# Kernel tuning notes

Hardware: AMD Instinct MI355X
Metric: run time of the kernel (lower is better)

Reference implementation:

```python
import jax, jax.numpy as jnp
import numpy as np

DIM = 256
HEAD_DIM = 64
NH = DIM // HEAD_DIM
PS = 2  # fine patch size
EPS = 1e-5


def _conv(x, w, b, stride, pad):
    y = jax.lax.conv_general_dilated(x, w, (stride, stride), ((pad, pad), (pad, pad)),
                                     dimension_numbers=('NCHW', 'OIHW', 'NCHW'))
    return y + b[None, :, None, None]


def _bn(x, g, b, m, v):
    s = g * jax.lax.rsqrt(v + EPS)
    return x * s[None, :, None, None] + (b - m * s)[None, :, None, None]


def setup_inputs() -> dict:
    key = jax.random.key(0)
    ks = jax.random.split(key, 24)
    C = DIM
    d = {}
    d['x'] = jax.random.normal(ks[0], (8, C, 64, 64), jnp.float32)
    # Downsample conv (C->C, k=4, s=2, p=1), torch OIHW layout
    d['w_down'] = jax.random.normal(ks[1], (C, C, 4, 4), jnp.float32) * 0.02
    d['b_down'] = jax.random.normal(ks[2], (C,), jnp.float32) * 0.02
    # coarse to_qkv Linear(64 -> 192), stored as [in, out]
    d['w_qkv_c'] = jax.random.normal(ks[3], (HEAD_DIM, 3 * HEAD_DIM), jnp.float32) * 0.05
    d['b_qkv_c'] = jax.random.normal(ks[4], (3 * HEAD_DIM,), jnp.float32) * 0.02
    # Upsample ConvTranspose2d (torch [in, out, kH, kW] layout)
    d['w_up'] = jax.random.normal(ks[5], (C, C, 4, 4), jnp.float32) * 0.02
    d['b_up'] = jax.random.normal(ks[6], (C,), jnp.float32) * 0.02
    # fine to_qkv Linear(64 -> 192)
    d['w_qkv_f'] = jax.random.normal(ks[7], (HEAD_DIM, 3 * HEAD_DIM), jnp.float32) * 0.05
    d['b_qkv_f'] = jax.random.normal(ks[8], (3 * HEAD_DIM,), jnp.float32) * 0.02
    # DWConv: depthwise 3x3 (groups=C) -> BN -> relu6 -> pointwise 1x1 -> BN -> relu6
    d['w_dw'] = jax.random.normal(ks[9], (C, 1, 3, 3), jnp.float32) * 0.1
    d['bn_dw_g'] = jax.random.uniform(ks[10], (C,), jnp.float32) * 0.5 + 0.75
    d['bn_dw_b'] = jax.random.normal(ks[11], (C,), jnp.float32) * 0.1
    d['bn_dw_m'] = jax.random.normal(ks[12], (C,), jnp.float32) * 0.1
    d['bn_dw_v'] = jax.random.uniform(ks[13], (C,), jnp.float32) + 0.5
    d['w_pw'] = jax.random.normal(ks[14], (C, C, 1, 1), jnp.float32) * 0.05
    d['bn_pw_g'] = jax.random.uniform(ks[15], (C,), jnp.float32) * 0.5 + 0.75
    d['bn_pw_b'] = jax.random.normal(ks[16], (C,), jnp.float32) * 0.1
    d['bn_pw_m'] = jax.random.normal(ks[17], (C,), jnp.float32) * 0.1
    d['bn_pw_v'] = jax.random.uniform(ks[18], (C,), jnp.float32) + 0.5
    return d


def reference(x, w_down, b_down, w_qkv_c, b_qkv_c, w_up, b_up, w_qkv_f, b_qkv_f,
              w_dw, bn_dw_g, bn_dw_b, bn_dw_m, bn_dw_v,
              w_pw, bn_pw_g, bn_pw_b, bn_pw_m, bn_pw_v):
    B, C, H, W = x.shape
    nh, hd = C // HEAD_DIM, HEAD_DIM
    scale = hd ** -0.5

    # ---- CoarseSelfAttention ----
    xd = _conv(x, w_down, b_down, 2, 1)           # [B,C,h,w]
    h, w = xd.shape[2], xd.shape[3]
    P = h * w
    tok = xd.reshape(B, nh, hd, P).transpose(0, 1, 3, 2)   # [B,nh,P,hd]
    q, k, v = jnp.split(tok @ w_qkv_c + b_qkv_c, 3, axis=-1)
    attn = jax.nn.softmax(jnp.einsum('bhqd,bhkd->bhqk', q, k) * scale, axis=-1)
    coarse_score = attn.sum(axis=-2)               # [B,nh,P]
    kf = max(1, P // 4)
    top_k = jax.lax.top_k(coarse_score, kf)[1]     # [B,nh,kf]
    out = jnp.einsum('bhqk,bhkd->bhqd', attn, v)
    out = out.transpose(0, 1, 3, 2).reshape(B, C, h, w)
    # ConvTranspose2d(k=4,s=2,p=1) as lhs-dilated conv with flipped/transposed kernel
    wt = jnp.flip(w_up, (2, 3)).transpose(1, 0, 2, 3)
    coarse = jax.lax.conv_general_dilated(out, wt, (1, 1), ((2, 2), (2, 2)),
                                          lhs_dilation=(2, 2),
                                          dimension_numbers=('NCHW', 'OIHW', 'NCHW'))
    coarse = coarse + b_up[None, :, None, None]
    # F.interpolate to (H,W) is identity here: upsample exactly restores HxW

    # ---- TopkSelfAttention ----
    ph, pw = H // PS, W // PS                      # ph*pw == P
    xh = coarse.reshape(B, nh, hd, ph, PS, pw, PS)
    patches = xh.transpose(0, 1, 2, 3, 5, 4, 6).reshape(B, nh, hd, ph * pw, PS, PS)
    idx = jnp.broadcast_to(top_k[:, :, None, :, None, None], (B, nh, hd, kf, PS, PS))
    sel = jnp.take_along_axis(patches, idx, axis=3)        # [B,nh,hd,kf,PS,PS]
    tokf = sel.reshape(B, nh, hd, kf, PS * PS).transpose(0, 1, 3, 4, 2)
    tokf = tokf.reshape(B, nh, kf * PS * PS, hd)
    qf, kk, vf = jnp.split(tokf @ w_qkv_f + b_qkv_f, 3, axis=-1)
    attnf = jax.nn.softmax(jnp.einsum('bhqd,bhkd->bhqk', qf, kk) * scale, axis=-1)
    outf = jnp.einsum('bhqk,bhkd->bhqd', attnf, vf)
    outf = outf.reshape(B, nh, kf, PS * PS, hd).transpose(0, 1, 2, 4, 3)
    outf = outf.reshape(B, nh, kf, hd, PS, PS)     # [B,nh,kf,hd,PS,PS]
    # scatter selected patches back into zeros (topk indices are unique per b,h)
    res = jnp.zeros((B, nh, ph * pw, hd, PS, PS), x.dtype)
    bi = jnp.arange(B)[:, None, None]
    hi = jnp.arange(nh)[None, :, None]
    res = res.at[bi, hi, top_k].set(outf)
    res = res.transpose(0, 1, 3, 2, 4, 5).reshape(B, nh, hd, ph, pw, PS, PS)
    region = res.transpose(0, 1, 2, 3, 5, 4, 6).reshape(B, C, H, W)

    y = coarse + region

    # ---- DWConv feed-forward ----
    yd = jax.lax.conv_general_dilated(y, w_dw, (1, 1), ((1, 1), (1, 1)),
                                      feature_group_count=C,
                                      dimension_numbers=('NCHW', 'OIHW', 'NCHW'))
    yd = jnp.clip(_bn(yd, bn_dw_g, bn_dw_b, bn_dw_m, bn_dw_v), 0.0, 6.0)
    yp = jax.lax.conv_general_dilated(yd, w_pw, (1, 1), ((0, 0), (0, 0)),
                                      dimension_numbers=('NCHW', 'OIHW', 'NCHW'))
    yp = jnp.clip(_bn(yp, bn_pw_g, bn_pw_b, bn_pw_m, bn_pw_v), 0.0, 6.0)
    return yp
```

## Files before the change

kernel.cpp:

```cpp
#include <hip/hip_runtime.h>
#include <cstdint>
#include <cstddef>


#define EPS_ 1e-5f

typedef short bf16x8_t __attribute__((ext_vector_type(8)));
typedef float f32x4_t __attribute__((ext_vector_type(4)));
#define MFMA16(a, b, c) __builtin_amdgcn_mfma_f32_16x16x32_bf16(a, b, c, 0, 0, 0)

__device__ __forceinline__ void cvt1(float f, unsigned short& h, unsigned short& l) {
  unsigned u = __float_as_uint(f);
  unsigned r = u + 0x7FFFu + ((u >> 16) & 1u);
  h = (unsigned short)(r >> 16);
  float lo = f - __uint_as_float(r & 0xFFFF0000u);
  l = (unsigned short)(__float_as_uint(lo) >> 16);
}
__device__ __forceinline__ unsigned cvtpack(float f) {
  unsigned short h, l;
  cvt1(f, h, l);
  return (unsigned)h | ((unsigned)l << 16);
}
__device__ __forceinline__ void cvt2(float f0, float f1, unsigned& hpack, unsigned& lpack) {
  unsigned u0 = __float_as_uint(f0), u1 = __float_as_uint(f1);
  unsigned r0 = u0 + 0x7FFFu + ((u0 >> 16) & 1u);
  unsigned r1 = u1 + 0x7FFFu + ((u1 >> 16) & 1u);
  hpack = (r0 >> 16) | (r1 & 0xFFFF0000u);
  float l0 = f0 - __uint_as_float(r0 & 0xFFFF0000u);
  float l1 = f1 - __uint_as_float(r1 & 0xFFFF0000u);
  lpack = (__float_as_uint(l0) >> 16) | (__float_as_uint(l1) & 0xFFFF0000u);
}
__device__ __forceinline__ unsigned pk_h(unsigned a, unsigned b) {
  return (a & 0xFFFFu) | (b << 16);
}
__device__ __forceinline__ unsigned pk_l(unsigned a, unsigned b) {
  return (a >> 16) | (b & 0xFFFF0000u);
}

__global__ __launch_bounds__(256) void k_pad_x(
    const float* __restrict__ x, unsigned* __restrict__ xphl) {
  const int plane = blockIdx.x;
  const float* src = x + (size_t)plane * 4096;
  unsigned* dst = xphl + (size_t)plane * 4488;
  for (int e = threadIdx.x; e < 4356; e += 256) {
    int r = e / 66, cc = e - r * 66;
    float v = 0.f;
    if (r >= 1 && r <= 64 && cc >= 1 && cc <= 64) v = src[(r - 1) * 64 + (cc - 1)];
    dst[r * 68 + cc] = cvtpack(v);
  }
}

__global__ __launch_bounds__(256) void k_cvt_wdown(
    const float* __restrict__ w, unsigned short* __restrict__ wh,
    unsigned short* __restrict__ wl) {
  int e = blockIdx.x * 256 + threadIdx.x;
  cvt1(w[e], wh[e], wl[e]);
}

__global__ __launch_bounds__(256) void k_cvt_wqkv(
    const float* __restrict__ wq, unsigned short* __restrict__ wh,
    unsigned short* __restrict__ wl) {
  int e = blockIdx.x * 256 + threadIdx.x;
  int col = e >> 6, d = e & 63;
  float f = wq[d * 192 + col];
  if (col < 64) f *= 0.125f;
  cvt1(f, wh[e], wl[e]);
}

__global__ __launch_bounds__(256) void k_cvt_wup(
    const float* __restrict__ w_up, unsigned short* __restrict__ wth,
    unsigned short* __restrict__ wtl) {
  int e = blockIdx.x * 256 + threadIdx.x;
  int kp = e & 1023, oc = (e >> 10) & 255, c = e >> 18;
  int tap = kp >> 8, ic = kp & 255;
  int tk = tap >> 1, txi = tap & 1;
  int ry = c >> 1, rx = c & 1;
  int ky = (1 - ry) + 2 * tk, kx = (1 - rx) + 2 * txi;
  cvt1(w_up[((size_t)(ic * 256 + oc) * 4 + ky) * 4 + kx], wth[e], wtl[e]);
}

__global__ __launch_bounds__(256) void k_cvt_wpw(
    const float* __restrict__ w, unsigned short* __restrict__ wh,
    unsigned short* __restrict__ wl) {
  int e = blockIdx.x * 256 + threadIdx.x;
  cvt1(w[e], wh[e], wl[e]);
}

__device__ __forceinline__ void mfma_chunk(
    const unsigned short (*Ah)[72], const unsigned short (*Al)[72],
    const unsigned short (*Bh)[72], const unsigned short (*Bl)[72],
    f32x4_t (&acc)[4], int wm, int lane) {
  const int l16 = lane & 15, quad = lane >> 4;
#pragma unroll
  for (int ks = 0; ks < 2; ++ks) {
    int ko = ks * 32 + quad * 8;
    bf16x8_t ah = *(const bf16x8_t*)&Ah[wm + l16][ko];
    bf16x8_t al = *(const bf16x8_t*)&Al[wm + l16][ko];
#pragma unroll
    for (int nt = 0; nt < 4; ++nt) {
      bf16x8_t bh = *(const bf16x8_t*)&Bh[nt * 16 + l16][ko];
      bf16x8_t bl = *(const bf16x8_t*)&Bl[nt * 16 + l16][ko];
      acc[nt] = MFMA16(ah, bh, acc[nt]);
      acc[nt] = MFMA16(ah, bl, acc[nt]);
      acc[nt] = MFMA16(al, bh, acc[nt]);
    }
  }
}

__device__ __forceinline__ void mfma_chunk_regB(
    const unsigned short (*Ah)[72], const unsigned short (*Al)[72],
    const bf16x8_t (&bh)[2][4], const bf16x8_t (&bl)[2][4],
    f32x4_t (&acc)[4], int wm, int lane) {
  const int l16 = lane & 15, quad = lane >> 4;
#pragma unroll
  for (int ks = 0; ks < 2; ++ks) {
    int ko = ks * 32 + quad * 8;
    bf16x8_t ah = *(const bf16x8_t*)&Ah[wm + l16][ko];
    bf16x8_t al = *(const bf16x8_t*)&Al[wm + l16][ko];
#pragma unroll
    for (int nt = 0; nt < 4; ++nt) {
      acc[nt] = MFMA16(ah, bh[ks][nt], acc[nt]);
      acc[nt] = MFMA16(ah, bl[ks][nt], acc[nt]);
      acc[nt] = MFMA16(al, bh[ks][nt], acc[nt]);
    }
  }
}

__device__ __forceinline__ void mfma_tile2x2(
    const unsigned short (*Ah)[72], const unsigned short (*Al)[72],
    const unsigned short (*Bh)[72], const unsigned short (*Bl)[72],
    f32x4_t (&acc)[2][2], int wm, int wn, int lane) {
  const int l16 = lane & 15, quad = lane >> 4;
#pragma unroll
  for (int ks = 0; ks < 2; ++ks) {
    int ko = ks * 32 + quad * 8;
    bf16x8_t ah[2], al[2];
#pragma unroll
    for (int mt = 0; mt < 2; ++mt) {
      ah[mt] = *(const bf16x8_t*)&Ah[wm + mt * 16 + l16][ko];
      al[mt] = *(const bf16x8_t*)&Al[wm + mt * 16 + l16][ko];
    }
#pragma unroll
    for (int nt = 0; nt < 2; ++nt) {
      bf16x8_t bh = *(const bf16x8_t*)&Bh[wn + nt * 16 + l16][ko];
      bf16x8_t bl = *(const bf16x8_t*)&Bl[wn + nt * 16 + l16][ko];
#pragma unroll
      for (int mt = 0; mt < 2; ++mt) {
        acc[mt][nt] = MFMA16(ah[mt], bh, acc[mt][nt]);
        acc[mt][nt] = MFMA16(ah[mt], bl, acc[mt][nt]);
        acc[mt][nt] = MFMA16(al[mt], bh, acc[mt][nt]);
      }
    }
  }
}

__device__ __forceinline__ void mfma_tile4x4(
    const unsigned short (*Ah)[72], const unsigned short (*Al)[72],
    const unsigned short (*Bh)[72], const unsigned short (*Bl)[72],
    f32x4_t (&acc)[4][4], int wm, int wn, int lane) {
  const int l16 = lane & 15, quad = lane >> 4;
#pragma unroll
  for (int ks = 0; ks < 2; ++ks) {
    int ko = ks * 32 + quad * 8;
    bf16x8_t ah[4], al[4];
#pragma unroll
    for (int mt = 0; mt < 4; ++mt) {
      ah[mt] = *(const bf16x8_t*)&Ah[wm + mt * 16 + l16][ko];
      al[mt] = *(const bf16x8_t*)&Al[wm + mt * 16 + l16][ko];
    }
#pragma unroll
    for (int nt = 0; nt < 4; ++nt) {
      bf16x8_t bh = *(const bf16x8_t*)&Bh[wn + nt * 16 + l16][ko];
      bf16x8_t bl = *(const bf16x8_t*)&Bl[wn + nt * 16 + l16][ko];
#pragma unroll
      for (int mt = 0; mt < 4; ++mt) {
        acc[mt][nt] = MFMA16(ah[mt], bh, acc[mt][nt]);
        acc[mt][nt] = MFMA16(ah[mt], bl, acc[mt][nt]);
        acc[mt][nt] = MFMA16(al[mt], bh, acc[mt][nt]);
      }
    }
  }
}

__global__ __launch_bounds__(256) void k_conv_down_mfma(
    const unsigned* __restrict__ xphl, const unsigned short* __restrict__ wdh,
    const unsigned short* __restrict__ wdl, const float* __restrict__ bias,
    unsigned* __restrict__ xdhl) {
  __shared__ unsigned short Ah[2][64][72], Al[2][64][72];
  __shared__ unsigned short Bh[2][64][72], Bl[2][64][72];
  const int t = threadIdx.x;
  const int pix0 = blockIdx.x * 64, oc0 = blockIdx.y * 64;
  const int bimg = pix0 >> 10, pos = pix0 & 1023;
  const int pl = t & 63, icg = t >> 6;
  const int rem = (pix0 + pl) & 1023;
  const int oy = rem >> 5, ox = rem & 31;
  const unsigned* xb = xphl + ((size_t)bimg * 256 + icg) * 4488 + (oy * 2) * 68 + ox * 2;
  const int wave = t >> 6, lane = t & 63, l16 = lane & 15, quad = lane >> 4;
  const int wm = (wave & 1) * 32, wn = (wave >> 1) * 32;
  const int ar = t >> 2, ac = (t & 3) * 16;
  const unsigned short* wra = wdh + (size_t)(oc0 + ar) * 4096 + ac;
  const unsigned short* wrl = wdl + (size_t)(oc0 + ar) * 4096 + ac;
  f32x4_t acc[2][2] = {};
  bf16x8_t a0, a1, a2, a3;
  uint2 u01[4], u23[4];
  a0 = *(const bf16x8_t*)(wra);
  a1 = *(const bf16x8_t*)(wra + 8);
  a2 = *(const bf16x8_t*)(wrl);
  a3 = *(const bf16x8_t*)(wrl + 8);
#pragma unroll
  for (int r = 0; r < 4; ++r) {
    u01[r] = *(const uint2*)(xb + r * 68);
    u23[r] = *(const uint2*)(xb + r * 68 + 2);
  }
  int cur = 0;
  for (int kb = 0; kb < 4096; kb += 64) {
    unsigned hp[8], lp[8];
#pragma unroll
    for (int r = 0; r < 4; ++r) {
      hp[2 * r]     = pk_h(u01[r].x, u01[r].y);
      lp[2 * r]     = pk_l(u01[r].x, u01[r].y);
      hp[2 * r + 1] = pk_h(u23[r].x, u23[r].y);
      lp[2 * r + 1] = pk_l(u23[r].x, u23[r].y);
    }
    *(bf16x8_t*)&Ah[cur][ar][ac] = a0;
    *(bf16x8_t*)&Ah[cur][ar][ac + 8] = a1;
    *(bf16x8_t*)&Al[cur][ar][ac] = a2;
    *(bf16x8_t*)&Al[cur][ar][ac + 8] = a3;
    *(uint4*)&Bh[cur][pl][icg * 16] = make_uint4(hp[0], hp[1], hp[2], hp[3]);
    *(uint4*)&Bh[cur][pl][icg * 16 + 8] = make_uint4(hp[4], hp[5], hp[6], hp[7]);
    *(uint4*)&Bl[cur][pl][icg * 16] = make_uint4(lp[0], lp[1], lp[2], lp[3]);
    *(uint4*)&Bl[cur][pl][icg * 16 + 8] = make_uint4(lp[4], lp[5], lp[6], lp[7]);
    if (kb + 64 < 4096) {
      xb += 4 * 4488;
      a0 = *(const bf16x8_t*)(wra + kb + 64);
      a1 = *(const bf16x8_t*)(wra + kb + 64 + 8);
      a2 = *(const bf16x8_t*)(wrl + kb + 64);
      a3 = *(const bf16x8_t*)(wrl + kb + 64 + 8);
#pragma unroll
      for (int r = 0; r < 4; ++r) {
        u01[r] = *(const uint2*)(xb + r * 68);
        u23[r] = *(const uint2*)(xb + r * 68 + 2);
      }
    }
    __syncthreads();
    mfma_tile2x2(Ah[cur], Al[cur], Bh[cur], Bl[cur], acc, wm, wn, lane);
    cur ^= 1;
  }
#pragma unroll
  for (int mt = 0; mt < 2; ++mt)
#pragma unroll
    for (int r = 0; r < 4; ++r) {
      int oc = oc0 + wm + mt * 16 + quad * 4 + r;
      float bv = bias[oc];
#pragma unroll
      for (int nt = 0; nt < 2; ++nt)
        xdhl[((size_t)(bimg * 256 + oc)) * 1024 + pos + wn + nt * 16 + l16] =
            cvtpack(acc[mt][nt][r] + bv);
    }
}

template <int MODE>
__global__ __launch_bounds__(256) void k_qkv_mfma(
    const unsigned* __restrict__ srcp, const float* __restrict__ srcf,
    const unsigned short* __restrict__ wh, const unsigned short* __restrict__ wl,
    const float* __restrict__ bq, const int* __restrict__ topk,
    unsigned short* __restrict__ qh, unsigned short* __restrict__ ql,
    unsigned short* __restrict__ kh, unsigned short* __restrict__ kl,
    unsigned short* __restrict__ vth, unsigned short* __restrict__ vtl) {
  __shared__ unsigned short Ah[64][72], Al[64][72];
  const int t = threadIdx.x;
  const int tok0 = blockIdx.x * 64;
  const int pair = blockIdx.y;
  const int b = pair >> 2, h = pair & 3;
  const int tokl = t & 63, dg = t >> 6;
  unsigned hp[8], lp[8];
  if (MODE == 0) {
    const unsigned* base = srcp + ((size_t)(b * 256 + h * 64 + dg * 16)) * 1024 + tok0 + tokl;
    unsigned u[16];
#pragma unroll
    for (int j = 0; j < 16; ++j) u[j] = base[(size_t)j * 1024];
#pragma unroll
    for (int j = 0; j < 8; ++j) {
      hp[j] = pk_h(u[2 * j], u[2 * j + 1]);
      lp[j] = pk_l(u[2 * j], u[2 * j + 1]);
    }
  } else {
    int tok = tok0 + tokl;
    int pp = topk[pair * 256 + (tok >> 2)];
    int py = (tok >> 1) & 1, px = tok & 1;
    int ry = (pp >> 5) * 2 + py, rx = (pp & 31) * 2 + px;
    const float* base = srcf + ((size_t)(b * 256 + h * 64 + dg * 16)) * 4096 + ry * 64 + rx;
    float fv[16];
#pragma unroll
    for (int j = 0; j < 16; ++j) fv[j] = base[(size_t)j * 4096];
#pragma unroll
    for (int j = 0; j < 8; ++j) cvt2(fv[2 * j], fv[2 * j + 1], hp[j], lp[j]);
  }
  *(uint4*)&Ah[tokl][dg * 16] = make_uint4(hp[0], hp[1], hp[2], hp[3]);
  *(uint4*)&Ah[tokl][dg * 16 + 8] = make_uint4(hp[4], hp[5], hp[6], hp[7]);
  *(uint4*)&Al[tokl][dg * 16] = make_uint4(lp[0], lp[1], lp[2], lp[3]);
  *(uint4*)&Al[tokl][dg * 16 + 8] = make_uint4(lp[4], lp[5], lp[6], lp[7]);
  __syncthreads();
  const int wave = t >> 6, lane = t & 63, l16 = lane & 15, quad = lane >> 4;
  f32x4_t acc[4][3] = {};
#pragma unroll
  for (int ks = 0; ks < 2; ++ks) {
    int ko = ks * 32 + quad * 8;
    bf16x8_t bh0[3], bl0[3];
#pragma unroll
    for (int nt = 0; nt < 3; ++nt) {
      int col = wave * 48 + nt * 16 + l16;
      bh0[nt] = *(const bf16x8_t*)(wh + col * 64 + ko);
      bl0[nt] = *(const bf16x8_t*)(wl + col * 64 + ko);
    }
#pragma unroll
    for (int mt = 0; mt < 4; ++mt) {
      bf16x8_t ah = *(const bf16x8_t*)&Ah[mt * 16 + l16][ko];
      bf16x8_t al = *(const bf16x8_t*)&Al[mt * 16 + l16][ko];
#pragma unroll
      for (int nt = 0; nt < 3; ++nt) {
        acc[mt][nt] = MFMA16(ah, bh0[nt], acc[mt][nt]);
        acc[mt][nt] = MFMA16(ah, bl0[nt], acc[mt][nt]);
        acc[mt][nt] = MFMA16(al, bh0[nt], acc[mt][nt]);
      }
    }
  }
#pragma unroll
  for (int nt = 0; nt < 3; ++nt) {
    int col = wave * 48 + nt * 16 + l16;
    float bqv = bq[col];
    if (col < 64) bqv *= 0.125f;
#pragma unroll
    for (int mt = 0; mt < 4; ++mt) {
#pragma unroll
      for (int r = 0; r < 4; ++r) {
        int tok = tok0 + mt * 16 + quad * 4 + r;
        float val = acc[mt][nt][r] + bqv;
        unsigned short hh, ll;
        cvt1(val, hh, ll);
        if (col < 64) {
          size_t o = ((size_t)pair * 1024 + tok) * 64 + col;
          qh[o] = hh; ql[o] = ll;
        } else if (col < 128) {
          size_t o = ((size_t)pair * 1024 + tok) * 64 + (col - 64);
          kh[o] = hh; kl[o] = ll;
        } else {
          size_t o = ((size_t)pair * 64 + (col - 128)) * 1024 + tok;
          vth[o] = hh; vtl[o] = ll;
        }
      }
    }
  }
}

__global__ __launch_bounds__(256, 2) void k_attn_coarse(
    const unsigned short* __restrict__ qh, const unsigned short* __restrict__ ql,
    const unsigned short* __restrict__ kh, const unsigned short* __restrict__ kl,
    const unsigned short* __restrict__ vth, const unsigned short* __restrict__ vtl,
    float* __restrict__ score, unsigned* __restrict__ outc) {
  __shared__ __align__(16) unsigned short Kb[2][64][72];
  __shared__ __align__(16) unsigned short Vb[2][64][72];
  __shared__ __align__(16) unsigned short Pb[2][64][72];
  __shared__ float mlW[4][2][64];
  __shared__ float mC[64], lC[64];
  __shared__ float colsum[1024];
  const int t = threadIdx.x;
  const int q0 = blockIdx.x * 64;
  const int pair = blockIdx.y;
  const int wave = t >> 6, lane = t & 63;
  const int l16 = lane & 15, quad = lane >> 4;
  const int wm = wave * 16;
  const int sr = t >> 3, skc = (t & 7) * 8;

  const size_t qbase = ((size_t)pair * 1024 + q0) * 64;
  bf16x8_t qh_r[2][4], ql_r[2][4];
#pragma unroll
  for (int ks = 0; ks < 2; ++ks)
#pragma unroll
    for (int nt = 0; nt < 4; ++nt) {
      int row = nt * 16 + l16, col = ks * 32 + quad * 8;
      qh_r[ks][nt] = *(const bf16x8_t*)(qh + qbase + (size_t)row * 64 + col);
      ql_r[ks][nt] = *(const bf16x8_t*)(ql + qbase + (size_t)row * 64 + col);
    }
#pragma unroll
  for (int i = 0; i < 4; ++i) colsum[t + i * 256] = 0.f;

  const size_t kmbase = (size_t)pair * 1024 * 64;
  const size_t vbase = (size_t)pair * 64 * 1024;

  bf16x8_t pk0[2], pk1[2];
#pragma unroll
  for (int i = 0; i < 2; ++i) {
    int r = sr + i * 32;
    pk0[i] = *(const bf16x8_t*)(kh + kmbase + (size_t)r * 64 + skc);
    pk1[i] = *(const bf16x8_t*)(kl + kmbase + (size_t)r * 64 + skc);
  }

  float mrun[4] = {-1e30f, -1e30f, -1e30f, -1e30f};
  float lrun[4] = {0.f, 0.f, 0.f, 0.f};
  for (int kb = 0; kb < 1024; kb += 64) {
    __syncthreads();
#pragma unroll
    for (int i = 0; i < 2; ++i) {
      int r = sr + i * 32;
      *(bf16x8_t*)&Kb[0][r][skc] = pk0[i];
      *(bf16x8_t*)&Kb[1][r][skc] = pk1[i];
    }
    if (kb + 64 < 1024) {
#pragma unroll
      for (int i = 0; i < 2; ++i) {
        int r = sr + i * 32;
        pk0[i] = *(const bf16x8_t*)(kh + kmbase + (size_t)(kb + 64 + r) * 64 + skc);
        pk1[i] = *(const bf16x8_t*)(kl + kmbase + (size_t)(kb + 64 + r) * 64 + skc);
      }
    }
    __syncthreads();
    f32x4_t acc[4] = {};
    mfma_chunk_regB(Kb[0], Kb[1], qh_r, ql_r, acc, wm, lane);
#pragma unroll
    for (int nt = 0; nt < 4; ++nt) {
      float m0 = fmaxf(fmaxf(acc[nt][0], acc[nt][1]), fmaxf(acc[nt][2], acc[nt][3]));
      m0 = fmaxf(m0, __shfl_xor(m0, 16));
      m0 = fmaxf(m0, __shfl_xor(m0, 32));
      float mn = fmaxf(mrun[nt], m0);
      float s0 = __expf(acc[nt][0] - mn) + __expf(acc[nt][1] - mn) +
                 __expf(acc[nt][2] - mn) + __expf(acc[nt][3] - mn);
      s0 += __shfl_xor(s0, 16);
      s0 += __shfl_xor(s0, 32);
      lrun[nt] = lrun[nt] * __expf(mrun[nt] - mn) + s0;
      mrun[nt] = mn;
    }
  }
  bf16x8_t pv0[2], pv1[2];
#pragma unroll
  for (int i = 0; i < 2; ++i) {
    int r = sr + i * 32;
    pk0[i] = *(const bf16x8_t*)(kh + kmbase + (size_t)r * 64 + skc);
    pk1[i] = *(const bf16x8_t*)(kl + kmbase + (size_t)r * 64 + skc);
    pv0[i] = *(const bf16x8_t*)(vth + vbase + (size_t)r * 1024 + skc);
    pv1[i] = *(const bf16x8_t*)(vtl + vbase + (size_t)r * 1024 + skc);
  }
  __syncthreads();
  if (quad == 0) {
#pragma unroll
    for (int nt = 0; nt < 4; ++nt) {
      mlW[wave][0][nt * 16 + l16] = mrun[nt];
      mlW[wave][1][nt * 16 + l16] = lrun[nt];
    }
  }
  __syncthreads();
  if (t < 64) {
    float m0 = mlW[0][0][t], m1 = mlW[1][0][t], m2 = mlW[2][0][t], m3 = mlW[3][0][t];
    float mm = fmaxf(fmaxf(m0, m1), fmaxf(m2, m3));
    float ll = mlW[0][1][t] * __expf(m0 - mm) + mlW[1][1][t] * __expf(m1 - mm) +
               mlW[2][1][t] * __expf(m2 - mm) + mlW[3][1][t] * __expf(m3 - mm);
    mC[t] = mm;
    lC[t] = 1.0f / ll;
  }
  __syncthreads();
  float mq[4], il[4];
#pragma unroll
  for (int nt = 0; nt < 4; ++nt) {
    mq[nt] = mC[nt * 16 + l16];
    il[nt] = lC[nt * 16 + l16];
  }

  f32x4_t accO[4] = {};
  for (int kb = 0; kb < 1024; kb += 64) {
    __syncthreads();
#pragma unroll
    for (int i = 0; i < 2; ++i) {
      int r = sr + i * 32;
      *(bf16x8_t*)&Kb[0][r][skc] = pk0[i];
      *(bf16x8_t*)&Kb[1][r][skc] = pk1[i];
      *(bf16x8_t*)&Vb[0][r][skc] = pv0[i];
      *(bf16x8_t*)&Vb[1][r][skc] = pv1[i];
    }
    if (kb + 64 < 1024) {
#pragma unroll
      for (int i = 0; i < 2; ++i) {
        int r = sr + i * 32;
        pk0[i] = *(const bf16x8_t*)(kh + kmbase + (size_t)(kb + 64 + r) * 64 + skc);
        pk1[i] = *(const bf16x8_t*)(kl + kmbase + (size_t)(kb + 64 + r) * 64 + skc);
        pv0[i] = *(const bf16x8_t*)(vth + vbase + (size_t)r * 1024 + kb + 64 + skc);
        pv1[i] = *(const bf16x8_t*)(vtl + vbase + (size_t)r * 1024 + kb + 64 + skc);
      }
    }
    __syncthreads();
    f32x4_t acc[4] = {};
    mfma_chunk_regB(Kb[0], Kb[1], qh_r, ql_r, acc, wm, lane);
    float P[4][4];
#pragma unroll
    for (int nt = 0; nt < 4; ++nt)
#pragma unroll
      for (int r = 0; r < 4; ++r) P[nt][r] = __expf(acc[nt][r] - mq[nt]) * il[nt];
#pragma unroll
    for (int r = 0; r < 4; ++r) {
      float cs = P[0][r] + P[1][r] + P[2][r] + P[3][r];
      cs += __shfl_xor(cs, 1);
      cs += __shfl_xor(cs, 2);
      cs += __shfl_xor(cs, 4);
      cs += __shfl_xor(cs, 8);
      if (l16 == 0) colsum[kb + wm + quad * 4 + r] += cs;
    }
#pragma unroll
    for (int nt = 0; nt < 4; ++nt) {
      unsigned h01, l01, h23, l23;
      cvt2(P[nt][0], P[nt][1], h01, l01);
      cvt2(P[nt][2], P[nt][3], h23, l23);
      *(uint2*)&Pb[0][nt * 16 + l16][wm + quad * 4] = make_uint2(h01, h23);
      *(uint2*)&Pb[1][nt * 16 + l16][wm + quad * 4] = make_uint2(l01, l23);
    }
    __syncthreads();
    mfma_chunk(Pb[0], Pb[1], Vb[0], Vb[1], accO, wm, lane);
  }
  __syncthreads();

#pragma unroll
  for (int i = 0; i < 4; ++i)
    atomicAdd(&score[pair * 1024 + t + i * 256], colsum[t + i * 256]);
  float (*Tr)[68] = reinterpret_cast<float(*)[68]>(&Pb[0][0][0]);
#pragma unroll
  for (int nt = 0; nt < 4; ++nt)
#pragma unroll
    for (int r = 0; r < 4; ++r)
      Tr[nt * 16 + l16][wm + quad * 4 + r] = accO[nt][r];
  __syncthreads();
  const int b = pair >> 2, h = pair & 3;
#pragma unroll
  for (int i = 0; i < 16; ++i) {
    int e = t + i * 256;
    int d = e >> 6, ql_ = e & 63;
    int pix = q0 + ql_;
    int iy = (pix >> 5) + 1, ix = (pix & 31) + 1;
    outc[((size_t)(b * 256 + h * 64 + d)) * 1156 + iy * 34 + ix] = cvtpack(Tr[d][ql_]);
  }
}

__global__ __launch_bounds__(256, 2) void k_attn_fine(
    const unsigned short* __restrict__ qh, const unsigned short* __restrict__ ql,
    const unsigned short* __restrict__ kh, const unsigned short* __restrict__ kl,
    const unsigned short* __restrict__ vth, const unsigned short* __restrict__ vtl,
    float* __restrict__ outf) {
  __shared__ __align__(16) unsigned short Kb[2][64][72];
  __shared__ __align__(16) unsigned short Vb[2][64][72];
  __shared__ __align__(16) unsigned short Pb[2][64][72];
  __shared__ float m_run[64], l_run[64], alphaS[64];
  __shared__ float mWc[4][64], sWc[4][64];
  const int t = threadIdx.x;
  const int q0 = blockIdx.x * 64;
  const int pair = blockIdx.y;
  const int wave = t >> 6, lane = t & 63;
  const int l16 = lane & 15, quad = lane >> 4;
  const int wm = wave * 16;
  const int sr = t >> 3, skc = (t & 7) * 8;

  const size_t qbase = ((size_t)pair * 1024 + q0) * 64;
  bf16x8_t qh_r[2][4], ql_r[2][4];
#pragma unroll
  for (int ks = 0; ks < 2; ++ks)
#pragma unroll
    for (int nt = 0; nt < 4; ++nt) {
      int row = nt * 16 + l16, col = ks * 32 + quad * 8;
      qh_r[ks][nt] = *(const bf16x8_t*)(qh + qbase + (size_t)row * 64 + col);
      ql_r[ks][nt] = *(const bf16x8_t*)(ql + qbase + (size_t)row * 64 + col);
    }
  if (t < 64) { m_run[t] = -1e30f; l_run[t] = 0.f; }

  const size_t kmbase = (size_t)pair * 1024 * 64;
  const size_t vbase = (size_t)pair * 64 * 1024;

  bf16x8_t pk0[2], pk1[2], pv0[2], pv1[2];
#pragma unroll
  for (int i = 0; i < 2; ++i) {
    int r = sr + i * 32;
    pk0[i] = *(const bf16x8_t*)(kh + kmbase + (size_t)r * 64 + skc);
    pk1[i] = *(const bf16x8_t*)(kl + kmbase + (size_t)r * 64 + skc);
    pv0[i] = *(const bf16x8_t*)(vth + vbase + (size_t)r * 1024 + skc);
    pv1[i] = *(const bf16x8_t*)(vtl + vbase + (size_t)r * 1024 + skc);
  }

  f32x4_t accO[4] = {};
  for (int kb = 0; kb < 1024; kb += 64) {
    __syncthreads();
#pragma unroll
    for (int i = 0; i < 2; ++i) {
      int r = sr + i * 32;
      *(bf16x8_t*)&Kb[0][r][skc] = pk0[i];
      *(bf16x8_t*)&Kb[1][r][skc] = pk1[i];
      *(bf16x8_t*)&Vb[0][r][skc] = pv0[i];
      *(bf16x8_t*)&Vb[1][r][skc] = pv1[i];
    }
    if (kb + 64 < 1024) {
#pragma unroll
      for (int i = 0; i < 2; ++i) {
        int r = sr + i * 32;
        pk0[i] = *(const bf16x8_t*)(kh + kmbase + (size_t)(kb + 64 + r) * 64 + skc);
        pk1[i] = *(const bf16x8_t*)(kl + kmbase + (size_t)(kb + 64 + r) * 64 + skc);
        pv0[i] = *(const bf16x8_t*)(vth + vbase + (size_t)r * 1024 + kb + 64 + skc);
        pv1[i] = *(const bf16x8_t*)(vtl + vbase + (size_t)r * 1024 + kb + 64 + skc);
      }
    }
    __syncthreads();
    f32x4_t acc[4] = {};
    mfma_chunk_regB(Kb[0], Kb[1], qh_r, ql_r, acc, wm, lane);
#pragma unroll
    for (int nt = 0; nt < 4; ++nt) {
      float m0 = fmaxf(fmaxf(acc[nt][0], acc[nt][1]), fmaxf(acc[nt][2], acc[nt][3]));
      m0 = fmaxf(m0, __shfl_xor(m0, 16));
      m0 = fmaxf(m0, __shfl_xor(m0, 32));
      if (quad == 0) mWc[wave][nt * 16 + l16] = m0;
    }
    __syncthreads();
    if (t < 64) {
      float mn = fmaxf(fmaxf(fmaxf(mWc[0][t], mWc[1][t]), fmaxf(mWc[2][t], mWc[3][t])),
                       m_run[t]);
      alphaS[t] = __expf(m_run[t] - mn);
      m_run[t] = mn;
    }
    __syncthreads();
    float P[4][4];
#pragma unroll
    for (int nt = 0; nt < 4; ++nt) {
      float mn = m_run[nt * 16 + l16];
#pragma unroll
      for (int r = 0; r < 4; ++r) P[nt][r] = __expf(acc[nt][r] - mn);
      float s0 = P[nt][0] + P[nt][1] + P[nt][2] + P[nt][3];
      s0 += __shfl_xor(s0, 16);
      s0 += __shfl_xor(s0, 32);
      if (quad == 0) sWc[wave][nt * 16 + l16] = s0;
      unsigned h01, l01, h23, l23;
      cvt2(P[nt][0], P[nt][1], h01, l01);
      cvt2(P[nt][2], P[nt][3], h23, l23);
      *(uint2*)&Pb[0][nt * 16 + l16][wm + quad * 4] = make_uint2(h01, h23);
      *(uint2*)&Pb[1][nt * 16 + l16][wm + quad * 4] = make_uint2(l01, l23);
    }
#pragma unroll
    for (int r = 0; r < 4; ++r) {
      float a = alphaS[wm + quad * 4 + r];
#pragma unroll
      for (int nt = 0; nt < 4; ++nt) accO[nt][r] *= a;
    }
    __syncthreads();
    if (t < 64)
      l_run[t] = l_run[t] * alphaS[t] + (sWc[0][t] + sWc[1][t] + sWc[2][t] + sWc[3][t]);
    mfma_chunk(Pb[0], Pb[1], Vb[0], Vb[1], accO, wm, lane);
  }
  __syncthreads();
#pragma unroll
  for (int r = 0; r < 4; ++r) {
    float invl = 1.0f / l_run[wm + quad * 4 + r];
    int qm = q0 + wm + quad * 4 + r;
#pragma unroll
    for (int nt = 0; nt < 4; ++nt)
      outf[((size_t)pair * 1024 + qm) * 64 + nt * 16 + l16] = accO[nt][r] * invl;
  }
}

__global__ __launch_bounds__(256) void k_topk(
    const float* __restrict__ score, int* __restrict__ idx) {
  __shared__ unsigned long long key[1024];
  const int pair = blockIdx.x;
  const int t = threadIdx.x;
#pragma unroll
  for (int j = 0; j < 4; ++j) {
    int i = t + j * 256;
    unsigned u = __float_as_uint(score[pair * 1024 + i]);
    u = u ^ ((u & 0x80000000u) ? 0xFFFFFFFFu : 0x80000000u);
    u = ~u;
    key[i] = ((unsigned long long)u << 32) | (unsigned)i;
  }
  __syncthreads();
  for (int k = 2; k <= 1024; k <<= 1) {
    for (int j = k >> 1; j > 0; j >>= 1) {
      for (int w = 0; w < 4; ++w) {
        int i = t + w * 256;
        int l = i ^ j;
        if (l > i) {
          bool up = ((i & k) == 0);
          unsigned long long a = key[i], b = key[l];
          if ((a > b) == up) { key[i] = b; key[l] = a; }
        }
      }
      __syncthreads();
    }
  }
  idx[pair * 256 + t] = (int)(key[t] & 0xFFFFFFFFu);
}

__global__ __launch_bounds__(256) void k_convT_mfma(
    const unsigned* __restrict__ inp, const unsigned short* __restrict__ wth,
    const unsigned short* __restrict__ wtl, const float* __restrict__ bias,
    float* __restrict__ out) {
  __shared__ unsigned short Ah[128][72], Al[128][72];
  __shared__ unsigned short Bh[128][72], Bl[128][72];
  const int t = threadIdx.x;
  const int pix0 = blockIdx.x * 128;
  const int oc0 = blockIdx.y * 128;
  const int cls = blockIdx.z;
  const int ry = cls >> 1, rx = cls & 1;
  const int b = pix0 >> 10;
  const int wave = t >> 6, lane = t & 63;
  const int l16 = lane & 15, quad = lane >> 4;
  const int wm = (wave & 1) * 64, wn = (wave >> 1) * 64;
  const int pl = t & 127, icg = t >> 7;
  const int remg = (pix0 + pl) & 1023;
  const int tyy = remg >> 5, txx = remg & 31;
  const int ar = t >> 1, ac = (t & 1) * 32;
  const size_t wbase = ((size_t)cls * 256 + oc0 + ar) * 1024 + ac;
  f32x4_t acc[4][4] = {};
  bf16x8_t awh[4], awl[4];
  unsigned u[32];
  {
    const int iy = tyy + ry + 1, ix = txx + rx + 1;
    const unsigned* p = inp + (size_t)(b * 256 + icg * 32) * 1156 + iy * 34 + ix;
#pragma unroll
    for (int j = 0; j < 32; ++j) u[j] = p[(size_t)j * 1156];
#pragma unroll
    for (int j = 0; j < 4; ++j) {
      awh[j] = *(const bf16x8_t*)(wth + wbase + j * 8);
      awl[j] = *(const bf16x8_t*)(wtl + wbase + j * 8);
    }
  }
  for (int kb = 0; kb < 1024; kb += 64) {
    unsigned hp[16], lpk[16];
#pragma unroll
    for (int j = 0; j < 16; ++j) {
      hp[j] = pk_h(u[2 * j], u[2 * j + 1]);
      lpk[j] = pk_l(u[2 * j], u[2 * j + 1]);
    }
    __syncthreads();
#pragma unroll
    for (int j = 0; j < 4; ++j) {
      *(bf16x8_t*)&Ah[ar][ac + j * 8] = awh[j];
      *(bf16x8_t*)&Al[ar][ac + j * 8] = awl[j];
    }
    {
      int kc = icg * 32;
      *(uint4*)&Bh[pl][kc] = make_uint4(hp[0], hp[1], hp[2], hp[3]);
      *(uint4*)&Bh[pl][kc + 8] = make_uint4(hp[4], hp[5], hp[6], hp[7]);
      *(uint4*)&Bh[pl][kc + 16] = make_uint4(hp[8], hp[9], hp[10], hp[11]);
      *(uint4*)&Bh[pl][kc + 24] = make_uint4(hp[12], hp[13], hp[14], hp[15]);
      *(uint4*)&Bl[pl][kc] = make_uint4(lpk[0], lpk[1], lpk[2], lpk[3]);
      *(uint4*)&Bl[pl][kc + 8] = make_uint4(lpk[4], lpk[5], lpk[6], lpk[7]);
      *(uint4*)&Bl[pl][kc + 16] = make_uint4(lpk[8], lpk[9], lpk[10], lpk[11]);
      *(uint4*)&Bl[pl][kc + 24] = make_uint4(lpk[12], lpk[13], lpk[14], lpk[15]);
    }
    if (kb + 64 < 1024) {
      const int kn = kb + 64;
      const int tap = kn >> 8, ic0 = kn & 255;
      const int tk = tap >> 1, txi = tap & 1;
      const int iy = tyy + ry + 1 - tk, ix = txx + rx + 1 - txi;
      const unsigned* p = inp + (size_t)(b * 256 + ic0 + icg * 32) * 1156 + iy * 34 + ix;
#pragma unroll
      for (int j = 0; j < 32; ++j) u[j] = p[(size_t)j * 1156];
#pragma unroll
      for (int j = 0; j < 4; ++j) {
        awh[j] = *(const bf16x8_t*)(wth + wbase + kn + j * 8);
        awl[j] = *(const bf16x8_t*)(wtl + wbase + kn + j * 8);
      }
    }
    __syncthreads();
    mfma_tile4x4(Ah, Al, Bh, Bl, acc, wm, wn, lane);
  }
#pragma unroll
  for (int mt = 0; mt < 4; ++mt)
#pragma unroll
    for (int r = 0; r < 4; ++r) {
      int oc = oc0 + wm + mt * 16 + quad * 4 + r;
      float bvs = bias[oc];
#pragma unroll
      for (int nt = 0; nt < 4; ++nt) {
        int pix = pix0 + wn + nt * 16 + l16;
        int rem2 = pix & 1023;
        int y = (rem2 >> 5) * 2 + ry, xx = (rem2 & 31) * 2 + rx;
        out[((size_t)(b * 256 + oc) * 64 + y) * 64 + xx] = acc[mt][nt][r] + bvs;
      }
    }
}

__global__ __launch_bounds__(256) void k_scatter(
    const float* __restrict__ outf, const int* __restrict__ idx,
    float* __restrict__ y) {
  int g = blockIdx.x * 256 + threadIdx.x;
  int pair = g >> 16;
  int rem = g & 65535;
  int tok = rem >> 6, d = rem & 63;
  int b = pair >> 2, h = pair & 3;
  int pp = idx[pair * 256 + (tok >> 2)];
  int py = (tok >> 1) & 1, px = tok & 1;
  int ry = (pp >> 5) * 2 + py, rx = (pp & 31) * 2 + px;
  y[((size_t)(b * 256 + h * 64 + d) * 64 + ry) * 64 + rx] += outf[g];
}

__global__ __launch_bounds__(256) void k_dwconv(
    const float* __restrict__ y, const float* __restrict__ wdw,
    const float* __restrict__ g, const float* __restrict__ bb,
    const float* __restrict__ m, const float* __restrict__ vv,
    unsigned* __restrict__ ydhl) {
  int gi = blockIdx.x * 256 + threadIdx.x;
  int x = gi & 63, yy = (gi >> 6) & 63, ch = (gi >> 12) & 255, b = gi >> 20;
  const float* plane = y + (size_t)(b * 256 + ch) * 4096;
  const float* wc = wdw + ch * 9;
  float s = 0.f;
#pragma unroll
  for (int ky = 0; ky < 3; ++ky) {
    int iy = yy + ky - 1;
    if (iy < 0 || iy >= 64) continue;
#pragma unroll
    for (int kx = 0; kx < 3; ++kx) {
      int ix = x + kx - 1;
      if (ix < 0 || ix >= 64) continue;
      s = fmaf(plane[iy * 64 + ix], wc[ky * 3 + kx], s);
    }
  }
  float sc = g[ch] * rsqrtf(vv[ch] + EPS_);
  float val = s * sc + (bb[ch] - m[ch] * sc);
  ydhl[gi] = cvtpack(fminf(fmaxf(val, 0.f), 6.f));
}

__global__ __launch_bounds__(256) void k_pw_mfma(
    const unsigned* __restrict__ ydhl, const unsigned short* __restrict__ wh,
    const unsigned short* __restrict__ wl, const float* __restrict__ g,
    const float* __restrict__ bb, const float* __restrict__ m,
    const float* __restrict__ vv, float* __restrict__ out) {
  __shared__ unsigned short Ah[128][72], Al[128][72];
  __shared__ unsigned short Bh[128][72], Bl[128][72];
  const int t = threadIdx.x;
  const int pix0 = blockIdx.x * 128;
  const int oc0 = blockIdx.y * 128;
  const int b = pix0 >> 12, pos0 = pix0 & 4095;
  const int wave = t >> 6, lane = t & 63;
  const int l16 = lane & 15, quad = lane >> 4;
  const int wm = (wave & 1) * 64, wn = (wave >> 1) * 64;
  const int pl = t & 127, icg = t >> 7;
  const int ar = t >> 1, ac = (t & 1) * 32;
  f32x4_t acc[4][4] = {};
  bf16x8_t awh[4], awl[4];
  unsigned u[32];
  {
    const unsigned* p = ydhl + (size_t)(b * 256 + icg * 32) * 4096 + pos0 + pl;
#pragma unroll
    for (int j = 0; j < 32; ++j) u[j] = p[(size_t)j * 4096];
#pragma unroll
    for (int j = 0; j < 4; ++j) {
      awh[j] = *(const bf16x8_t*)(wh + (size_t)(oc0 + ar) * 256 + ac + j * 8);
      awl[j] = *(const bf16x8_t*)(wl + (size_t)(oc0 + ar) * 256 + ac + j * 8);
    }
  }
  for (int kb = 0; kb < 256; kb += 64) {
    unsigned hp[16], lpk[16];
#pragma unroll
    for (int j = 0; j < 16; ++j) {
      hp[j] = pk_h(u[2 * j], u[2 * j + 1]);
      lpk[j] = pk_l(u[2 * j], u[2 * j + 1]);
    }
    __syncthreads();
#pragma unroll
    for (int j = 0; j < 4; ++j) {
      *(bf16x8_t*)&Ah[ar][ac + j * 8] = awh[j];
      *(bf16x8_t*)&Al[ar][ac + j * 8] = awl[j];
    }
    {
      int kc = icg * 32;
      *(uint4*)&Bh[pl][kc] = make_uint4(hp[0], hp[1], hp[2], hp[3]);
      *(uint4*)&Bh[pl][kc + 8] = make_uint4(hp[4], hp[5], hp[6], hp[7]);
      *(uint4*)&Bh[pl][kc + 16] = make_uint4(hp[8], hp[9], hp[10], hp[11]);
      *(uint4*)&Bh[pl][kc + 24] = make_uint4(hp[12], hp[13], hp[14], hp[15]);
      *(uint4*)&Bl[pl][kc] = make_uint4(lpk[0], lpk[1], lpk[2], lpk[3]);
      *(uint4*)&Bl[pl][kc + 8] = make_uint4(lpk[4], lpk[5], lpk[6], lpk[7]);
      *(uint4*)&Bl[pl][kc + 16] = make_uint4(lpk[8], lpk[9], lpk[10], lpk[11]);
      *(uint4*)&Bl[pl][kc + 24] = make_uint4(lpk[12], lpk[13], lpk[14], lpk[15]);
    }
    if (kb + 64 < 256) {
      const int kn = kb + 64;
      const unsigned* p = ydhl + (size_t)(b * 256 + kn + icg * 32) * 4096 + pos0 + pl;
#pragma unroll
      for (int j = 0; j < 32; ++j) u[j] = p[(size_t)j * 4096];
#pragma unroll
      for (int j = 0; j < 4; ++j) {
        awh[j] = *(const bf16x8_t*)(wh + (size_t)(oc0 + ar) * 256 + kn + ac + j * 8);
        awl[j] = *(const bf16x8_t*)(wl + (size_t)(oc0 + ar) * 256 + kn + ac + j * 8);
      }
    }
    __syncthreads();
    mfma_tile4x4(Ah, Al, Bh, Bl, acc, wm, wn, lane);
  }
#pragma unroll
  for (int mt = 0; mt < 4; ++mt)
#pragma unroll
    for (int r = 0; r < 4; ++r) {
      int oc = oc0 + wm + mt * 16 + quad * 4 + r;
      float sc = g[oc] * rsqrtf(vv[oc] + EPS_);
      float off = bb[oc] - m[oc] * sc;
#pragma unroll
      for (int nt = 0; nt < 4; ++nt) {
        int pix = pos0 + wn + nt * 16 + l16;
        float val = fminf(fmaxf(acc[mt][nt][r] * sc + off, 0.f), 6.f);
        out[(size_t)(b * 256 + oc) * 4096 + pix] = val;
      }
    }
}

extern "C" void kernel_launch(void* const* d_in, const int* in_sizes, int n_in,
                              void* d_out, int out_size, void* d_ws, size_t ws_size,
                              hipStream_t stream) {
  (void)in_sizes; (void)n_in; (void)out_size; (void)ws_size;
  const float* x       = (const float*)d_in[0];
  const float* w_down  = (const float*)d_in[1];
  const float* b_down  = (const float*)d_in[2];
  const float* w_qkv_c = (const float*)d_in[3];
  const float* b_qkv_c = (const float*)d_in[4];
  const float* w_up    = (const float*)d_in[5];
  const float* b_up    = (const float*)d_in[6];
  const float* w_qkv_f = (const float*)d_in[7];
  const float* b_qkv_f = (const float*)d_in[8];
  const float* w_dw    = (const float*)d_in[9];
  const float* bn_dw_g = (const float*)d_in[10];
  const float* bn_dw_b = (const float*)d_in[11];
  const float* bn_dw_m = (const float*)d_in[12];
  const float* bn_dw_v = (const float*)d_in[13];
  const float* w_pw    = (const float*)d_in[14];
  const float* bn_pw_g = (const float*)d_in[15];
  const float* bn_pw_b = (const float*)d_in[16];
  const float* bn_pw_m = (const float*)d_in[17];
  const float* bn_pw_v = (const float*)d_in[18];

  float* ws = (float*)d_ws;
  unsigned*       xphl   = (unsigned*)ws;
  unsigned*       ydhl   = (unsigned*)ws;
  unsigned short* qh     = (unsigned short*)(ws + 33554432);
  unsigned short* ql     = (unsigned short*)(ws + 34603008);
  unsigned short* kh     = (unsigned short*)(ws + 35651584);
  unsigned short* kl     = (unsigned short*)(ws + 36700160);
  unsigned short* vth    = (unsigned short*)(ws + 37748736);
  unsigned short* vtl    = (unsigned short*)(ws + 38797312);
  unsigned*       xdhl   = (unsigned*)(ws + 39845888);
  unsigned*       outcphl= (unsigned*)(ws + 41943040);
  float*          coarse = ws + 44310528;
  float*          outf   = ws + 52699136;
  float*          score  = ws + 54796288;
  unsigned short* wdh    = (unsigned short*)(ws + 54829056);
  unsigned short* wdl    = (unsigned short*)(ws + 55353344);
  unsigned short* wt_hi  = (unsigned short*)(ws + 55877632);
  unsigned short* wt_lo  = (unsigned short*)(ws + 56401920);
  unsigned short* wpw_hi = (unsigned short*)(ws + 56926208);
  unsigned short* wpw_lo = (unsigned short*)(ws + 56958976);
  unsigned short* wqh_c  = (unsigned short*)(ws + 56991744);
  unsigned short* wql_c  = (unsigned short*)(ws + 56997888);
  unsigned short* wqh_f  = (unsigned short*)(ws + 57004032);
  unsigned short* wql_f  = (unsigned short*)(ws + 57010176);
  int*            idx    = (int*)(ws + 57016320);

  hipMemsetAsync(score, 0, 32768 * sizeof(float), stream);
  hipMemsetAsync(outcphl, 0, (size_t)2367488 * sizeof(unsigned), stream);
  k_pad_x<<<2048, 256, 0, stream>>>(x, xphl);
  k_cvt_wdown<<<4096, 256, 0, stream>>>(w_down, wdh, wdl);
  k_cvt_wqkv<<<48, 256, 0, stream>>>(w_qkv_c, wqh_c, wql_c);
  k_cvt_wqkv<<<48, 256, 0, stream>>>(w_qkv_f, wqh_f, wql_f);
  k_cvt_wup<<<4096, 256, 0, stream>>>(w_up, wt_hi, wt_lo);
  k_cvt_wpw<<<256, 256, 0, stream>>>(w_pw, wpw_hi, wpw_lo);

  k_conv_down_mfma<<<dim3(128, 4), 256, 0, stream>>>(xphl, wdh, wdl, b_down, xdhl);
  k_qkv_mfma<0><<<dim3(16, 32), 256, 0, stream>>>(xdhl, nullptr, wqh_c, wql_c, b_qkv_c,
                                                  nullptr, qh, ql, kh, kl, vth, vtl);
  k_attn_coarse<<<dim3(16, 32), 256, 0, stream>>>(qh, ql, kh, kl, vth, vtl, score, outcphl);
  k_topk<<<32, 256, 0, stream>>>(score, idx);
  k_convT_mfma<<<dim3(64, 2, 4), 256, 0, stream>>>(outcphl, wt_hi, wt_lo, b_up, coarse);

  k_qkv_mfma<1><<<dim3(16, 32), 256, 0, stream>>>(nullptr, coarse, wqh_f, wql_f, b_qkv_f,
                                                  idx, qh, ql, kh, kl, vth, vtl);
  k_attn_fine<<<dim3(16, 32), 256, 0, stream>>>(qh, ql, kh, kl, vth, vtl, outf);
  k_scatter<<<8192, 256, 0, stream>>>(outf, idx, coarse);
  k_dwconv<<<32768, 256, 0, stream>>>(coarse, w_dw, bn_dw_g, bn_dw_b, bn_dw_m, bn_dw_v, ydhl);
  k_pw_mfma<<<dim3(256, 2), 256, 0, stream>>>(ydhl, wpw_hi, wpw_lo, bn_pw_g, bn_pw_b,
                                              bn_pw_m, bn_pw_v, (float*)d_out);
}
```

Baseline: 575.9 us.

## Load downsample-conv B operand directly into MFMA fragment registers, bypassing LDS

The downsample conv kernel no longer stages the input-patch (B) operand through shared memory. Each lane gathers exactly the bf16 hi/lo fragments it needs for its MFMA tiles straight from global memory and packs them in registers. This removes the B LDS stores and reads and halves shared memory use, which may raise occupancy. In exchange, waves sharing the same pixel columns load that data redundantly from global memory, register pressure goes up, and the global access pattern is less coalesced.

```diff
diff --git a/kernel.cpp b/kernel.cpp
--- a/kernel.cpp
+++ b/kernel.cpp
@@ -126,10 +126,10 @@
   }
 }
 
-__device__ __forceinline__ void mfma_tile2x2(
+__device__ __forceinline__ void mfma_tile2x2_regB(
     const unsigned short (*Ah)[72], const unsigned short (*Al)[72],
-    const unsigned short (*Bh)[72], const unsigned short (*Bl)[72],
-    f32x4_t (&acc)[2][2], int wm, int wn, int lane) {
+    const bf16x8_t (&bh)[2][2], const bf16x8_t (&bl)[2][2],
+    f32x4_t (&acc)[2][2], int wm, int lane) {
   const int l16 = lane & 15, quad = lane >> 4;
 #pragma unroll
   for (int ks = 0; ks < 2; ++ks) {
@@ -142,13 +142,11 @@
     }
 #pragma unroll
     for (int nt = 0; nt < 2; ++nt) {
-      bf16x8_t bh = *(const bf16x8_t*)&Bh[wn + nt * 16 + l16][ko];
-      bf16x8_t bl = *(const bf16x8_t*)&Bl[wn + nt * 16 + l16][ko];
 #pragma unroll
       for (int mt = 0; mt < 2; ++mt) {
-        acc[mt][nt] = MFMA16(ah[mt], bh, acc[mt][nt]);
-        acc[mt][nt] = MFMA16(ah[mt], bl, acc[mt][nt]);
-        acc[mt][nt] = MFMA16(al[mt], bh, acc[mt][nt]);
+        acc[mt][nt] = MFMA16(ah[mt], bh[ks][nt], acc[mt][nt]);
+        acc[mt][nt] = MFMA16(ah[mt], bl[ks][nt], acc[mt][nt]);
+        acc[mt][nt] = MFMA16(al[mt], bh[ks][nt], acc[mt][nt]);
       }
     }
   }
@@ -187,63 +185,80 @@
     const unsigned short* __restrict__ wdl, const float* __restrict__ bias,
     unsigned* __restrict__ xdhl) {
   __shared__ unsigned short Ah[2][64][72], Al[2][64][72];
-  __shared__ unsigned short Bh[2][64][72], Bl[2][64][72];
   const int t = threadIdx.x;
   const int pix0 = blockIdx.x * 64, oc0 = blockIdx.y * 64;
   const int bimg = pix0 >> 10, pos = pix0 & 1023;
-  const int pl = t & 63, icg = t >> 6;
-  const int rem = (pix0 + pl) & 1023;
-  const int oy = rem >> 5, ox = rem & 31;
-  const unsigned* xb = xphl + ((size_t)bimg * 256 + icg) * 4488 + (oy * 2) * 68 + ox * 2;
   const int wave = t >> 6, lane = t & 63, l16 = lane & 15, quad = lane >> 4;
   const int wm = (wave & 1) * 32, wn = (wave >> 1) * 32;
   const int ar = t >> 2, ac = (t & 3) * 16;
   const unsigned short* wra = wdh + (size_t)(oc0 + ar) * 4096 + ac;
   const unsigned short* wrl = wdl + (size_t)(oc0 + ar) * 4096 + ac;
+  const unsigned* bp[2];
+#pragma unroll
+  for (int nt = 0; nt < 2; ++nt) {
+    int rem = (pix0 + wn + nt * 16 + l16) & 1023;
+    int oy = rem >> 5, ox = rem & 31;
+    bp[nt] = xphl + ((size_t)bimg * 256 + (quad >> 1)) * 4488 +
+             (size_t)(oy * 2 + (quad & 1) * 2) * 68 + ox * 2;
+  }
   f32x4_t acc[2][2] = {};
   bf16x8_t a0, a1, a2, a3;
-  uint2 u01[4], u23[4];
+  uint2 bu[2][2][4];
   a0 = *(const bf16x8_t*)(wra);
   a1 = *(const bf16x8_t*)(wra + 8);
   a2 = *(const bf16x8_t*)(wrl);
   a3 = *(const bf16x8_t*)(wrl + 8);
 #pragma unroll
-  for (int r = 0; r < 4; ++r) {
-    u01[r] = *(const uint2*)(xb + r * 68);
-    u23[r] = *(const uint2*)(xb + r * 68 + 2);
-  }
+  for (int nt = 0; nt < 2; ++nt)
+#pragma unroll
+    for (int ks = 0; ks < 2; ++ks) {
+      const unsigned* q = bp[nt] + (size_t)(ks * 2) * 4488;
+      bu[nt][ks][0] = *(const uint2*)(q);
+      bu[nt][ks][1] = *(const uint2*)(q + 2);
+      bu[nt][ks][2] = *(const uint2*)(q + 68);
+      bu[nt][ks][3] = *(const uint2*)(q + 70);
+    }
   int cur = 0;
   for (int kb = 0; kb < 4096; kb += 64) {
-    unsigned hp[8], lp[8];
-#pragma unroll
-    for (int r = 0; r < 4; ++r) {
-      hp[2 * r]     = pk_h(u01[r].x, u01[r].y);
-      lp[2 * r]     = pk_l(u01[r].x, u01[r].y);
-      hp[2 * r + 1] = pk_h(u23[r].x, u23[r].y);
-      lp[2 * r + 1] = pk_l(u23[r].x, u23[r].y);
-    }
+    bf16x8_t bhf[2][2], blf[2][2];
+#pragma unroll
+    for (int nt = 0; nt < 2; ++nt)
+#pragma unroll
+      for (int ks = 0; ks < 2; ++ks) {
+        unsigned hp[4], lp[4];
+#pragma unroll
+        for (int j = 0; j < 4; ++j) {
+          hp[j] = pk_h(bu[nt][ks][j].x, bu[nt][ks][j].y);
+          lp[j] = pk_l(bu[nt][ks][j].x, bu[nt][ks][j].y);
+        }
+        uint4 h4 = make_uint4(hp[0], hp[1], hp[2], hp[3]);
+        uint4 l4 = make_uint4(lp[0], lp[1], lp[2], lp[3]);
+        bhf[ks][nt] = *(const bf16x8_t*)&h4;
+        blf[ks][nt] = *(const bf16x8_t*)&l4;
+      }
     *(bf16x8_t*)&Ah[cur][ar][ac] = a0;
     *(bf16x8_t*)&Ah[cur][ar][ac + 8] = a1;
     *(bf16x8_t*)&Al[cur][ar][ac] = a2;
     *(bf16x8_t*)&Al[cur][ar][ac + 8] = a3;
-    *(uint4*)&Bh[cur][pl][icg * 16] = make_uint4(hp[0], hp[1], hp[2], hp[3]);
-    *(uint4*)&Bh[cur][pl][icg * 16 + 8] = make_uint4(hp[4], hp[5], hp[6], hp[7]);
-    *(uint4*)&Bl[cur][pl][icg * 16] = make_uint4(lp[0], lp[1], lp[2], lp[3]);
-    *(uint4*)&Bl[cur][pl][icg * 16 + 8] = make_uint4(lp[4], lp[5], lp[6], lp[7]);
     if (kb + 64 < 4096) {
-      xb += 4 * 4488;
       a0 = *(const bf16x8_t*)(wra + kb + 64);
       a1 = *(const bf16x8_t*)(wra + kb + 64 + 8);
       a2 = *(const bf16x8_t*)(wrl + kb + 64);
       a3 = *(const bf16x8_t*)(wrl + kb + 64 + 8);
-#pragma unroll
-      for (int r = 0; r < 4; ++r) {
-        u01[r] = *(const uint2*)(xb + r * 68);
-        u23[r] = *(const uint2*)(xb + r * 68 + 2);
-      }
-    }
-    __syncthreads();
-    mfma_tile2x2(Ah[cur], Al[cur], Bh[cur], Bl[cur], acc, wm, wn, lane);
+      const int kc4 = (kb >> 4) + 4;
+#pragma unroll
+      for (int nt = 0; nt < 2; ++nt)
+#pragma unroll
+        for (int ks = 0; ks < 2; ++ks) {
+          const unsigned* q = bp[nt] + (size_t)(kc4 + ks * 2) * 4488;
+          bu[nt][ks][0] = *(const uint2*)(q);
+          bu[nt][ks][1] = *(const uint2*)(q + 2);
+          bu[nt][ks][2] = *(const uint2*)(q + 68);
+          bu[nt][ks][3] = *(const uint2*)(q + 70);
+        }
+    }
+    __syncthreads();
+    mfma_tile2x2_regB(Ah[cur], Al[cur], bhf, blf, acc, wm, lane);
     cur ^= 1;
   }
 #pragma unroll
```

Measured after the change: 583.2 us. No clear change (+1.3%).
